# Kernel tuning notes

Measured on AMD Instinct MI355X. Metric: run time of the kernel, lower is better.

The kernel has to match this reference:

```python
import jax, jax.numpy as jnp
import numpy as np

N_NODES = 100000
N_EDGES = 1600000
F_IN, F_HID, F_OUT = 256, 128, 32


def setup_inputs() -> dict:
    key = jax.random.key(0)
    k1, k2, k3, k4 = jax.random.split(key, 4)
    x = jax.random.normal(k1, (N_NODES, F_IN), dtype=jnp.float32)
    edge_index = jax.random.randint(k2, (2, N_EDGES), 0, N_NODES, dtype=jnp.int64)
    W1 = jax.random.normal(k3, (F_IN, F_HID), dtype=jnp.float32) * (1.0 / np.sqrt(F_IN))
    b1 = jnp.zeros((F_HID,), dtype=jnp.float32)
    W2 = jax.random.normal(k4, (F_HID, F_OUT), dtype=jnp.float32) * (1.0 / np.sqrt(F_HID))
    b2 = jnp.zeros((F_OUT,), dtype=jnp.float32)
    return {"x": x, "edge_index": edge_index, "W1": W1, "b1": b1, "W2": W2, "b2": b2}


def _gcn_norm(edge_index, num_nodes):
    # Add self-loops, then symmetric normalization deg^-1/2[src] * deg^-1/2[dst].
    loops = jnp.arange(num_nodes, dtype=edge_index.dtype)
    src = jnp.concatenate([edge_index[0], loops])
    dst = jnp.concatenate([edge_index[1], loops])
    deg = jax.ops.segment_sum(jnp.ones_like(dst, dtype=jnp.float32), dst,
                              num_segments=num_nodes)
    dinv = jnp.where(deg > 0, jax.lax.rsqrt(deg), 0.0)
    norm = dinv[src] * dinv[dst]  # [E + N]
    return src, dst, norm


def _gcn_conv(h, src, dst, norm, num_nodes):
    # h already linearly transformed. Gather sources, scale, scatter-add to dst.
    msgs = h[src] * norm[:, None]
    return jax.ops.segment_sum(msgs, dst, num_segments=num_nodes)


def reference(x, edge_index, W1, b1, W2, b2):
    n = x.shape[0]
    src, dst, norm = _gcn_norm(edge_index, n)
    # Layer 1: linear -> normalized scatter-add -> bias -> relu
    h = _gcn_conv(x @ W1, src, dst, norm, n) + b1
    h = jax.nn.relu(h)
    # F.dropout with training=False (eval mode) is identity.
    # Layer 2
    out = _gcn_conv(h @ W2, src, dst, norm, n) + b2
    return jax.nn.log_softmax(out, axis=1)
```

## Files before the change

kernel.cpp:

```cpp
#include <hip/hip_runtime.h>

#define N_NODES 100000
#define N_EDGES 1600000
#define F_IN 256
#define F_HID 128
#define F_OUT 32
#define NBUCK 391
#define BIN_BLOCKS 512
#define EDGES_PER_BIN 3125

typedef unsigned short ushort_t;
typedef unsigned int uint_t;

using short8  = __attribute__((ext_vector_type(8))) short;
using floatx4 = __attribute__((ext_vector_type(4))) float;

__device__ __forceinline__ ushort_t f2bf(float f) {
    uint_t u = __float_as_uint(f);
    u += 0x7fff + ((u >> 16) & 1);
    return (ushort_t)(u >> 16);
}
__device__ __forceinline__ float bf_lo(uint_t u) { return __uint_as_float(u << 16); }
__device__ __forceinline__ float bf_hi(uint_t u) { return __uint_as_float(u & 0xffff0000u); }
__device__ __forceinline__ uint_t bfpack_trunc(float a, float b) {
    return __builtin_amdgcn_perm(__float_as_uint(b), __float_as_uint(a), 0x07060302u);
}

__global__ __launch_bounds__(256) void histwt_kernel(const int* __restrict__ ei,
                                                     int* __restrict__ bucket_cnt,
                                                     const float* __restrict__ W1,
                                                     const float* __restrict__ W2,
                                                     ushort_t* __restrict__ W1T,
                                                     ushort_t* __restrict__ W2T) {
    __shared__ int h[NBUCK];
    if (blockIdx.x < BIN_BLOCKS) {
        for (int i = threadIdx.x; i < NBUCK; i += 256) h[i] = 0;
        __syncthreads();
        int gid = blockIdx.x * 256 + threadIdx.x;
        for (int e = gid; e < N_EDGES; e += BIN_BLOCKS * 256)
            atomicAdd(&h[ei[N_EDGES + e] >> 8], 1);
        __syncthreads();
        for (int i = threadIdx.x; i < NBUCK; i += 256) {
            int c = h[i];
            if (c) atomicAdd(&bucket_cnt[i], c);
        }
    } else {
        int t = (blockIdx.x - BIN_BLOCKS) * 256 + threadIdx.x;
#pragma unroll
        for (int j = 0; j < 4; j++) {
            int e = j * 8192 + t;
            int n = e >> 8, k = e & 255;
            W1T[e] = f2bf(W1[k * F_HID + n]);
        }
        if (t < 4096) {
            int n = t >> 7, k = t & 127;
            W2T[t] = f2bf(W2[k * F_OUT + n]);
        }
    }
}

__global__ __launch_bounds__(512) void scan_kernel(const int* __restrict__ bucket_cnt,
                                                   int* __restrict__ bucket_base,
                                                   int* __restrict__ bucket_cursor,
                                                   int* __restrict__ offs) {
    __shared__ int s[512];
    int t = threadIdx.x;
    int own = (t < NBUCK) ? bucket_cnt[t] : 0;
    s[t] = own;
    __syncthreads();
    for (int off = 1; off < 512; off <<= 1) {
        int v = (t >= off) ? s[t - off] : 0;
        __syncthreads();
        s[t] += v;
        __syncthreads();
    }
    if (t < NBUCK) {
        int ex = s[t] - own;
        bucket_base[t] = ex;
        bucket_cursor[t] = ex;
    }
    if (t == 0) {
        bucket_base[NBUCK] = N_EDGES;
        offs[N_NODES] = N_EDGES;
    }
}

__global__ __launch_bounds__(256) void bin_kernel(const int* __restrict__ ei,
                                                  int* __restrict__ bucket_cursor,
                                                  int2* __restrict__ binned) {
    __shared__ int h[NBUCK];
    __shared__ int base[NBUCK];
    const int t = threadIdx.x;
    const int beg = blockIdx.x * EDGES_PER_BIN;
    const int end = beg + EDGES_PER_BIN;
    for (int i = t; i < NBUCK; i += 256) h[i] = 0;
    __syncthreads();
    for (int e = beg + t; e < end; e += 256) atomicAdd(&h[ei[N_EDGES + e] >> 8], 1);
    __syncthreads();
    for (int i = t; i < NBUCK; i += 256) {
        int c = h[i];
        base[i] = c ? atomicAdd(&bucket_cursor[i], c) : 0;
        h[i] = 0;
    }
    __syncthreads();
    for (int e = beg + t; e < end; e += 256) {
        int s = ei[e], d = ei[N_EDGES + e];
        int bk = d >> 8;
        int p = base[bk] + atomicAdd(&h[bk], 1);
        binned[p] = make_int2(s, d);
    }
}

__global__ __launch_bounds__(256) void build_kernel(const int2* __restrict__ binned,
                                                    const int* __restrict__ bucket_base,
                                                    int* __restrict__ offs,
                                                    int* __restrict__ csr,
                                                    float* __restrict__ dinv,
                                                    int* __restrict__ degarr) {
    __shared__ int h[256];
    __shared__ int sc[256];
    __shared__ int cur[256];
    const int b = blockIdx.x, t = threadIdx.x;
    const int beg = bucket_base[b];
    const int end = bucket_base[b + 1];
    h[t] = 0;
    __syncthreads();
    for (int j = beg + t; j < end; j += 256) {
        int2 p = binned[j];
        atomicAdd(&h[p.y & 255], 1);
    }
    __syncthreads();
    int deg = h[t];
    sc[t] = deg;
    __syncthreads();
    for (int off = 1; off < 256; off <<= 1) {
        int v = (t >= off) ? sc[t - off] : 0;
        __syncthreads();
        sc[t] += v;
        __syncthreads();
    }
    int excl = sc[t] - deg;
    cur[t] = excl;
    int node = b * 256 + t;
    if (node < N_NODES) {
        offs[node] = beg + excl;
        dinv[node] = rsqrtf((float)deg + 1.0f);
        degarr[node] = deg;
    }
    __syncthreads();
    for (int j = beg + t; j < end; j += 256) {
        int2 p = binned[j];
        int pos = atomicAdd(&cur[p.y & 255], 1);
        csr[beg + pos] = p.x;
    }
}

__global__ __launch_bounds__(256) void pack_kernel(int* __restrict__ csr,
                                                   const int* __restrict__ degarr) {
    int i = blockIdx.x * 256 + threadIdx.x;
    if (i >= N_EDGES / 4) return;
    int4 c = ((int4*)csr)[i];
    c.x |= degarr[c.x] << 20;
    c.y |= degarr[c.y] << 20;
    c.z |= degarr[c.z] << 20;
    c.w |= degarr[c.w] << 20;
    ((int4*)csr)[i] = c;
}

__global__ __launch_bounds__(512) void gemm1_kernel(const float* __restrict__ x,
                                                    const ushort_t* __restrict__ W1T,
                                                    ushort_t* __restrict__ h0bf) {
    __shared__ ushort_t Bst[F_HID][F_IN + 8];
    const int tid = threadIdx.x;
    const int rbase = blockIdx.x * 128;
    const int w = tid >> 6;
    const int lane = tid & 63;
    const int q = lane >> 4;
    const int nloc = lane & 15;

#pragma unroll
    for (int j = 0; j < 8; j++) {
        int f = j * 512 + tid;
        int n = f >> 5, kg = f & 31;
        uint4 v = ((const uint4*)(W1T + n * F_IN))[kg];
        *(uint4*)(&Bst[n][kg * 8]) = v;
    }
    __syncthreads();

    const int rowA = rbase + w * 16 + nloc;
    const bool okA = rowA < N_NODES;
    const float* ap = x + (size_t)rowA * F_IN + q * 8;

    floatx4 acc[8];
#pragma unroll
    for (int t = 0; t < 8; t++) acc[t] = (floatx4){0.f, 0.f, 0.f, 0.f};

#pragma unroll
    for (int k0 = 0; k0 < F_IN; k0 += 32) {
        float4 f0 = make_float4(0.f, 0.f, 0.f, 0.f);
        float4 f1 = make_float4(0.f, 0.f, 0.f, 0.f);
        if (okA) {
            f0 = *(const float4*)(ap + k0);
            f1 = *(const float4*)(ap + k0 + 4);
        }
        uint4 au;
        au.x = bfpack_trunc(f0.x, f0.y);
        au.y = bfpack_trunc(f0.z, f0.w);
        au.z = bfpack_trunc(f1.x, f1.y);
        au.w = bfpack_trunc(f1.z, f1.w);
        short8 a = *(short8*)&au;
#pragma unroll
        for (int t = 0; t < 8; t++) {
            short8 b = *(const short8*)(&Bst[t * 16 + nloc][k0 + q * 8]);
            acc[t] = __builtin_amdgcn_mfma_f32_16x16x32_bf16(a, b, acc[t], 0, 0, 0);
        }
    }

#pragma unroll
    for (int reg = 0; reg < 4; reg++) {
        int rowD = rbase + w * 16 + q * 4 + reg;
        if (rowD < N_NODES) {
            ushort_t* op = h0bf + (size_t)rowD * F_HID + nloc;
#pragma unroll
            for (int t = 0; t < 8; t++) op[t * 16] = f2bf(acc[t][reg]);
        }
    }
}

__global__ __launch_bounds__(256) void gather128(const ushort_t* __restrict__ h0bf,
                                                 const int* __restrict__ offs,
                                                 const int* __restrict__ csr,
                                                 const float* __restrict__ dinv,
                                                 ushort_t* __restrict__ aggbf) {
    const int node = blockIdx.x * 8 + (threadIdx.x >> 5);
    const int l = threadIdx.x & 31;
    const int sub = l >> 4;
    const int fl = l & 15;
    const float dn = dinv[node];
    const uint4* rowbase = (const uint4*)h0bf;

    uint4 sv = rowbase[(size_t)node * 16 + fl];
    float s = (sub == 0) ? dn * dn : 0.f;
    float a[8];
    a[0] = bf_lo(sv.x) * s; a[1] = bf_hi(sv.x) * s;
    a[2] = bf_lo(sv.y) * s; a[3] = bf_hi(sv.y) * s;
    a[4] = bf_lo(sv.z) * s; a[5] = bf_hi(sv.z) * s;
    a[6] = bf_lo(sv.w) * s; a[7] = bf_hi(sv.w) * s;

    const int beg = offs[node], end = offs[node + 1];
    for (int j = beg; j < end; j += 16) {
        uint_t w[8];
        float nn[8];
        uint4 r[8];
#pragma unroll
        for (int k = 0; k < 8; k++) w[k] = ((const uint_t*)csr)[j + 2 * k + sub];
#pragma unroll
        for (int k = 0; k < 8; k++) {
            bool v = (j + 2 * k + sub) < end;
            int src = v ? (int)(w[k] & 0xFFFFFu) : 0;
            nn[k] = v ? rsqrtf((float)(w[k] >> 20) + 1.0f) * dn : 0.f;
            r[k] = rowbase[(size_t)src * 16 + fl];
        }
#pragma unroll
        for (int k = 0; k < 8; k++) {
            float n = nn[k];
            a[0] += bf_lo(r[k].x) * n; a[1] += bf_hi(r[k].x) * n;
            a[2] += bf_lo(r[k].y) * n; a[3] += bf_hi(r[k].y) * n;
            a[4] += bf_lo(r[k].z) * n; a[5] += bf_hi(r[k].z) * n;
            a[6] += bf_lo(r[k].w) * n; a[7] += bf_hi(r[k].w) * n;
        }
    }
#pragma unroll
    for (int i = 0; i < 8; i++) a[i] += __shfl_xor(a[i], 16);
    if (sub == 0) {
        uint4 p;
        p.x = (uint_t)f2bf(a[0]) | ((uint_t)f2bf(a[1]) << 16);
        p.y = (uint_t)f2bf(a[2]) | ((uint_t)f2bf(a[3]) << 16);
        p.z = (uint_t)f2bf(a[4]) | ((uint_t)f2bf(a[5]) << 16);
        p.w = (uint_t)f2bf(a[6]) | ((uint_t)f2bf(a[7]) << 16);
        ((uint4*)aggbf)[(size_t)node * 16 + fl] = p;
    }
}

__global__ __launch_bounds__(256) void gemm2_kernel(const ushort_t* __restrict__ aggbf,
                                                    const float* __restrict__ b1,
                                                    const ushort_t* __restrict__ W2T,
                                                    ushort_t* __restrict__ h2bf) {
    __shared__ ushort_t Bs[F_OUT][F_HID + 8];
    __shared__ float b1s[F_HID];
    const int tid = threadIdx.x;
    const int rbase = blockIdx.x * 64;
    const int w = tid >> 6;
    const int lane = tid & 63;
    const int q = lane >> 4;
    const int nloc = lane & 15;

    if (tid < F_HID) b1s[tid] = b1[tid];
#pragma unroll
    for (int jj = 0; jj < 2; jj++) {
        int f = jj * 256 + tid;
        int n = f >> 4, kg = f & 15;
        uint4 v = ((const uint4*)(W2T + n * F_HID))[kg];
        *(uint4*)(&Bs[n][kg * 8]) = v;
    }
    __syncthreads();

    const int rowA = rbase + w * 16 + nloc;
    const bool okA = rowA < N_NODES;

    floatx4 acc[2];
    acc[0] = (floatx4){0.f, 0.f, 0.f, 0.f};
    acc[1] = (floatx4){0.f, 0.f, 0.f, 0.f};

#pragma unroll
    for (int k0 = 0; k0 < F_HID; k0 += 32) {
        int kk = k0 + q * 8;
        uint4 av = make_uint4(0, 0, 0, 0);
        if (okA) av = *(const uint4*)(aggbf + (size_t)rowA * F_HID + kk);
        float4 bb0 = *(const float4*)(&b1s[kk]);
        float4 bb1 = *(const float4*)(&b1s[kk + 4]);
        uint4 au;
        au.x = bfpack_trunc(fmaxf(bf_lo(av.x) + bb0.x, 0.f), fmaxf(bf_hi(av.x) + bb0.y, 0.f));
        au.y = bfpack_trunc(fmaxf(bf_lo(av.y) + bb0.z, 0.f), fmaxf(bf_hi(av.y) + bb0.w, 0.f));
        au.z = bfpack_trunc(fmaxf(bf_lo(av.z) + bb1.x, 0.f), fmaxf(bf_hi(av.z) + bb1.y, 0.f));
        au.w = bfpack_trunc(fmaxf(bf_lo(av.w) + bb1.z, 0.f), fmaxf(bf_hi(av.w) + bb1.w, 0.f));
        short8 a = *(short8*)&au;
#pragma unroll
        for (int t = 0; t < 2; t++) {
            short8 b = *(const short8*)(&Bs[t * 16 + nloc][kk]);
            acc[t] = __builtin_amdgcn_mfma_f32_16x16x32_bf16(a, b, acc[t], 0, 0, 0);
        }
    }
#pragma unroll
    for (int reg = 0; reg < 4; reg++) {
        int rowD = rbase + w * 16 + q * 4 + reg;
        if (rowD < N_NODES) {
            ushort_t* op = h2bf + (size_t)rowD * F_OUT + nloc;
            op[0]  = f2bf(acc[0][reg]);
            op[16] = f2bf(acc[1][reg]);
        }
    }
}

__global__ __launch_bounds__(256) void gather32_lsm(const ushort_t* __restrict__ h2bf,
                                                    const int* __restrict__ offs,
                                                    const int* __restrict__ csr,
                                                    const float* __restrict__ dinv,
                                                    const float* __restrict__ b2,
                                                    float* __restrict__ out) {
    const int node = blockIdx.x * 8 + (threadIdx.x >> 5);
    const int l = threadIdx.x & 31;
    const int sub = l >> 2;
    const int fl = l & 3;
    const float dn = dinv[node];
    const uint4* rowbase = (const uint4*)h2bf;

    uint4 sv = rowbase[(size_t)node * 4 + fl];
    float s = (sub == 0) ? dn * dn : 0.f;
    float a[8];
    a[0] = bf_lo(sv.x) * s; a[1] = bf_hi(sv.x) * s;
    a[2] = bf_lo(sv.y) * s; a[3] = bf_hi(sv.y) * s;
    a[4] = bf_lo(sv.z) * s; a[5] = bf_hi(sv.z) * s;
    a[6] = bf_lo(sv.w) * s; a[7] = bf_hi(sv.w) * s;

    const int beg = offs[node], end = offs[node + 1];
    for (int j = beg; j < end; j += 16) {
        uint_t w[2];
        float nn[2];
        uint4 r[2];
#pragma unroll
        for (int k = 0; k < 2; k++) w[k] = ((const uint_t*)csr)[j + 8 * k + sub];
#pragma unroll
        for (int k = 0; k < 2; k++) {
            bool v = (j + 8 * k + sub) < end;
            int src = v ? (int)(w[k] & 0xFFFFFu) : 0;
            nn[k] = v ? rsqrtf((float)(w[k] >> 20) + 1.0f) * dn : 0.f;
            r[k] = rowbase[(size_t)src * 4 + fl];
        }
#pragma unroll
        for (int k = 0; k < 2; k++) {
            float n = nn[k];
            a[0] += bf_lo(r[k].x) * n; a[1] += bf_hi(r[k].x) * n;
            a[2] += bf_lo(r[k].y) * n; a[3] += bf_hi(r[k].y) * n;
            a[4] += bf_lo(r[k].z) * n; a[5] += bf_hi(r[k].z) * n;
            a[6] += bf_lo(r[k].w) * n; a[7] += bf_hi(r[k].w) * n;
        }
    }
#pragma unroll
    for (int i = 0; i < 8; i++) {
        a[i] += __shfl_xor(a[i], 4);
        a[i] += __shfl_xor(a[i], 8);
        a[i] += __shfl_xor(a[i], 16);
    }
    float4 bb0 = ((const float4*)b2)[fl * 2];
    float4 bb1 = ((const float4*)b2)[fl * 2 + 1];
    a[0] += bb0.x; a[1] += bb0.y; a[2] += bb0.z; a[3] += bb0.w;
    a[4] += bb1.x; a[5] += bb1.y; a[6] += bb1.z; a[7] += bb1.w;

    float m = a[0];
#pragma unroll
    for (int i = 1; i < 8; i++) m = fmaxf(m, a[i]);
    m = fmaxf(m, __shfl_xor(m, 1));
    m = fmaxf(m, __shfl_xor(m, 2));
    float es = 0.f;
#pragma unroll
    for (int i = 0; i < 8; i++) es += __expf(a[i] - m);
    es += __shfl_xor(es, 1);
    es += __shfl_xor(es, 2);
    float lse = m + __logf(es);

    if (sub == 0) {
        float4 o0 = make_float4(a[0] - lse, a[1] - lse, a[2] - lse, a[3] - lse);
        float4 o1 = make_float4(a[4] - lse, a[5] - lse, a[6] - lse, a[7] - lse);
        float4* op = (float4*)(out + (size_t)node * F_OUT);
        op[fl * 2] = o0;
        op[fl * 2 + 1] = o1;
    }
}

extern "C" void kernel_launch(void* const* d_in, const int* in_sizes, int n_in,
                              void* d_out, int out_size, void* d_ws, size_t ws_size,
                              hipStream_t stream) {
    const float* x  = (const float*)d_in[0];
    const int*   ei = (const int*)d_in[1];
    const float* W1 = (const float*)d_in[2];
    const float* b1 = (const float*)d_in[3];
    const float* W2 = (const float*)d_in[4];
    const float* b2 = (const float*)d_in[5];
    float* out = (float*)d_out;

    float* ws = (float*)d_ws;
    float*    dinv          = ws;
    int*      offs          = (int*)(ws + 100096);
    int*      bucket_cnt    = (int*)(ws + 200224);
    int*      bucket_base   = (int*)(ws + 200736);
    int*      bucket_cursor = (int*)(ws + 201248);
    int*      degarr        = (int*)(ws + 201760);
    int*      csr           = (int*)(ws + 301856);
    ushort_t* W1T           = (ushort_t*)(ws + 1901856);
    ushort_t* W2T           = (ushort_t*)(ws + 1918240);
    ushort_t* h0bf          = (ushort_t*)(ws + 1920288);
    ushort_t* aggbf         = (ushort_t*)(ws + 8320288);
    ushort_t* h2bf          = (ushort_t*)(ws + 14720288);
    int2*     binned        = (int2*)aggbf;

    hipMemsetAsync(bucket_cnt, 0, 512 * sizeof(int), stream);
    histwt_kernel<<<BIN_BLOCKS + 32, 256, 0, stream>>>(ei, bucket_cnt, W1, W2, W1T, W2T);
    scan_kernel<<<1, 512, 0, stream>>>(bucket_cnt, bucket_base, bucket_cursor, offs);
    bin_kernel<<<BIN_BLOCKS, 256, 0, stream>>>(ei, bucket_cursor, binned);
    build_kernel<<<NBUCK, 256, 0, stream>>>(binned, bucket_base, offs, csr, dinv, degarr);
    pack_kernel<<<(N_EDGES / 4 + 255) / 256, 256, 0, stream>>>(csr, degarr);
    gemm1_kernel<<<(N_NODES + 127) / 128, 512, 0, stream>>>(x, W1T, h0bf);
    gather128<<<N_NODES / 8, 256, 0, stream>>>(h0bf, offs, csr, dinv, aggbf);
    gemm2_kernel<<<(N_NODES + 63) / 64, 256, 0, stream>>>(aggbf, b1, W2T, h2bf);
    gather32_lsm<<<N_NODES / 8, 256, 0, stream>>>(h2bf, offs, csr, dinv, b2, out);
}
```

Before: 349.5 us.

## Split hidden features into two 64-wide halves and gather each separately

The first-layer hidden table is split column-wise into two 64-feature bf16 tables, and the layer-1 aggregation runs as two gather passes over those tables. Each half-table is 12.8 MB rather than 25.6 MB, so the random row gathers have a better chance of hitting in L2 or the last-level cache. The cost is a second pass over the CSR indices and degree normalisation, plus an extra kernel launch. gemm1 and gemm2 are adapted to write and read the split layout.

Result: no change. 350.9 us (+0.4%).

```diff
diff --git a/kernel.cpp b/kernel.cpp
--- a/kernel.cpp
+++ b/kernel.cpp
@@ -169,7 +169,8 @@
 
 __global__ __launch_bounds__(512) void gemm1_kernel(const float* __restrict__ x,
                                                     const ushort_t* __restrict__ W1T,
-                                                    ushort_t* __restrict__ h0bf) {
+                                                    ushort_t* __restrict__ h0a,
+                                                    ushort_t* __restrict__ h0b) {
     __shared__ ushort_t Bst[F_HID][F_IN + 8];
     const int tid = threadIdx.x;
     const int rbase = blockIdx.x * 128;
@@ -220,26 +221,29 @@
     for (int reg = 0; reg < 4; reg++) {
         int rowD = rbase + w * 16 + q * 4 + reg;
         if (rowD < N_NODES) {
-            ushort_t* op = h0bf + (size_t)rowD * F_HID + nloc;
-#pragma unroll
-            for (int t = 0; t < 8; t++) op[t * 16] = f2bf(acc[t][reg]);
-        }
-    }
-}
-
-__global__ __launch_bounds__(256) void gather128(const ushort_t* __restrict__ h0bf,
-                                                 const int* __restrict__ offs,
-                                                 const int* __restrict__ csr,
-                                                 const float* __restrict__ dinv,
-                                                 ushort_t* __restrict__ aggbf) {
+            ushort_t* opA = h0a + (size_t)rowD * 64 + nloc;
+            ushort_t* opB = h0b + (size_t)rowD * 64 + nloc;
+#pragma unroll
+            for (int t = 0; t < 4; t++) opA[t * 16] = f2bf(acc[t][reg]);
+#pragma unroll
+            for (int t = 4; t < 8; t++) opB[(t - 4) * 16] = f2bf(acc[t][reg]);
+        }
+    }
+}
+
+__global__ __launch_bounds__(256) void gather64(const ushort_t* __restrict__ tab,
+                                                const int* __restrict__ offs,
+                                                const int* __restrict__ csr,
+                                                const float* __restrict__ dinv,
+                                                ushort_t* __restrict__ outt) {
     const int node = blockIdx.x * 8 + (threadIdx.x >> 5);
     const int l = threadIdx.x & 31;
-    const int sub = l >> 4;
-    const int fl = l & 15;
+    const int sub = l >> 3;
+    const int fl = l & 7;
     const float dn = dinv[node];
-    const uint4* rowbase = (const uint4*)h0bf;
-
-    uint4 sv = rowbase[(size_t)node * 16 + fl];
+    const uint4* rowbase = (const uint4*)tab;
+
+    uint4 sv = rowbase[(size_t)node * 8 + fl];
     float s = (sub == 0) ? dn * dn : 0.f;
     float a[8];
     a[0] = bf_lo(sv.x) * s; a[1] = bf_hi(sv.x) * s;
@@ -249,20 +253,20 @@
 
     const int beg = offs[node], end = offs[node + 1];
     for (int j = beg; j < end; j += 16) {
-        uint_t w[8];
-        float nn[8];
-        uint4 r[8];
-#pragma unroll
-        for (int k = 0; k < 8; k++) w[k] = ((const uint_t*)csr)[j + 2 * k + sub];
-#pragma unroll
-        for (int k = 0; k < 8; k++) {
-            bool v = (j + 2 * k + sub) < end;
+        uint_t w[4];
+        float nn[4];
+        uint4 r[4];
+#pragma unroll
+        for (int k = 0; k < 4; k++) w[k] = ((const uint_t*)csr)[j + 4 * k + sub];
+#pragma unroll
+        for (int k = 0; k < 4; k++) {
+            bool v = (j + 4 * k + sub) < end;
             int src = v ? (int)(w[k] & 0xFFFFFu) : 0;
             nn[k] = v ? rsqrtf((float)(w[k] >> 20) + 1.0f) * dn : 0.f;
-            r[k] = rowbase[(size_t)src * 16 + fl];
-        }
-#pragma unroll
-        for (int k = 0; k < 8; k++) {
+            r[k] = rowbase[(size_t)src * 8 + fl];
+        }
+#pragma unroll
+        for (int k = 0; k < 4; k++) {
             float n = nn[k];
             a[0] += bf_lo(r[k].x) * n; a[1] += bf_hi(r[k].x) * n;
             a[2] += bf_lo(r[k].y) * n; a[3] += bf_hi(r[k].y) * n;
@@ -271,18 +275,22 @@
         }
     }
 #pragma unroll
-    for (int i = 0; i < 8; i++) a[i] += __shfl_xor(a[i], 16);
+    for (int i = 0; i < 8; i++) {
+        a[i] += __shfl_xor(a[i], 8);
+        a[i] += __shfl_xor(a[i], 16);
+    }
     if (sub == 0) {
         uint4 p;
         p.x = (uint_t)f2bf(a[0]) | ((uint_t)f2bf(a[1]) << 16);
         p.y = (uint_t)f2bf(a[2]) | ((uint_t)f2bf(a[3]) << 16);
         p.z = (uint_t)f2bf(a[4]) | ((uint_t)f2bf(a[5]) << 16);
         p.w = (uint_t)f2bf(a[6]) | ((uint_t)f2bf(a[7]) << 16);
-        ((uint4*)aggbf)[(size_t)node * 16 + fl] = p;
-    }
-}
-
-__global__ __launch_bounds__(256) void gemm2_kernel(const ushort_t* __restrict__ aggbf,
+        ((uint4*)outt)[(size_t)node * 8 + fl] = p;
+    }
+}
+
+__global__ __launch_bounds__(256) void gemm2_kernel(const ushort_t* __restrict__ aggA,
+                                                    const ushort_t* __restrict__ aggB,
                                                     const float* __restrict__ b1,
                                                     const ushort_t* __restrict__ W2T,
                                                     ushort_t* __restrict__ h2bf) {
@@ -315,8 +323,10 @@
 #pragma unroll
     for (int k0 = 0; k0 < F_HID; k0 += 32) {
         int kk = k0 + q * 8;
+        const ushort_t* at = (k0 < 64) ? aggA : aggB;
+        int kloc = (k0 < 64) ? kk : kk - 64;
         uint4 av = make_uint4(0, 0, 0, 0);
-        if (okA) av = *(const uint4*)(aggbf + (size_t)rowA * F_HID + kk);
+        if (okA) av = *(const uint4*)(at + (size_t)rowA * 64 + kloc);
         float4 bb0 = *(const float4*)(&b1s[kk]);
         float4 bb1 = *(const float4*)(&b1s[kk + 4]);
         uint4 au;
@@ -439,10 +449,12 @@
     int*      csr           = (int*)(ws + 301856);
     ushort_t* W1T           = (ushort_t*)(ws + 1901856);
     ushort_t* W2T           = (ushort_t*)(ws + 1918240);
-    ushort_t* h0bf          = (ushort_t*)(ws + 1920288);
-    ushort_t* aggbf         = (ushort_t*)(ws + 8320288);
+    ushort_t* h0a           = (ushort_t*)(ws + 1920288);
+    ushort_t* h0b           = (ushort_t*)(ws + 5120288);
+    ushort_t* aggA          = (ushort_t*)(ws + 8320288);
+    ushort_t* aggB          = (ushort_t*)(ws + 11520288);
     ushort_t* h2bf          = (ushort_t*)(ws + 14720288);
-    int2*     binned        = (int2*)aggbf;
+    int2*     binned        = (int2*)aggA;
 
     hipMemsetAsync(bucket_cnt, 0, 512 * sizeof(int), stream);
     histwt_kernel<<<BIN_BLOCKS + 32, 256, 0, stream>>>(ei, bucket_cnt, W1, W2, W1T, W2T);
@@ -450,8 +462,9 @@
     bin_kernel<<<BIN_BLOCKS, 256, 0, stream>>>(ei, bucket_cursor, binned);
     build_kernel<<<NBUCK, 256, 0, stream>>>(binned, bucket_base, offs, csr, dinv, degarr);
     pack_kernel<<<(N_EDGES / 4 + 255) / 256, 256, 0, stream>>>(csr, degarr);
-    gemm1_kernel<<<(N_NODES + 127) / 128, 512, 0, stream>>>(x, W1T, h0bf);
-    gather128<<<N_NODES / 8, 256, 0, stream>>>(h0bf, offs, csr, dinv, aggbf);
-    gemm2_kernel<<<(N_NODES + 63) / 64, 256, 0, stream>>>(aggbf, b1, W2T, h2bf);
+    gemm1_kernel<<<(N_NODES + 127) / 128, 512, 0, stream>>>(x, W1T, h0a, h0b);
+    gather64<<<N_NODES / 8, 256, 0, stream>>>(h0a, offs, csr, dinv, aggA);
+    gather64<<<N_NODES / 8, 256, 0, stream>>>(h0b, offs, csr, dinv, aggB);
+    gemm2_kernel<<<(N_NODES + 63) / 64, 256, 0, stream>>>(aggA, aggB, b1, W2T, h2bf);
     gather32_lsm<<<N_NODES / 8, 256, 0, stream>>>(h2bf, offs, csr, dinv, b2, out);
 }
```
